# Optimization experiments

Hardware: AMD Instinct MI355X
Metric: run time of the kernel (lower is better)

The kernel has to match this reference:

```python
import jax, jax.numpy as jnp
import numpy as np

L_IN, L_FREQ, L_OUT = 128, 64, 64
C_IN, C_OUT, T_DIM = 64, 64, 256
SPIN = 1

# ---------- self-contained spin-weighted SHT (MW sampling), replacing s2fft ----------

def _mw_thetas(L, extended):
    n = 2 * L - 1 if extended else L
    return (2 * np.arange(n) + 1) * np.pi / (2 * L - 1)

def _wigner_d_stack(L, thetas, n):
    # d^l_{m,n}(theta) = <l,m| exp(-i theta Jy) |l,n>, computed via eigh of the
    # Hermitian angular-momentum operator Jy. Output (ntheta, L, 2L-1), m at col L-1+m.
    nth = len(thetas)
    out = np.zeros((nth, L, 2 * L - 1), dtype=np.float64)
    for l in range(abs(n), L):
        dim = 2 * l + 1
        m = np.arange(-l, l).astype(np.float64)
        ap = np.sqrt(l * (l + 1.0) - m * (m + 1.0))
        Jy = np.zeros((dim, dim), dtype=np.complex128)
        i = np.arange(dim - 1)
        Jy[i + 1, i] = -0.5j * ap
        Jy[i, i + 1] = 0.5j * ap
        lam, V = np.linalg.eigh(Jy)
        coeff = V * np.conj(V[l + n, :])[None, :]
        phases = np.exp(-1j * np.outer(lam, thetas))
        out[:, l, L - 1 - l:L + l] = (coeff @ phases).T.real
    return out

def _mw_quad_weights(L):
    # per-theta weights on the mirror-extended grid: q_t = (1/(2L-1)) sum_k w(k) e^{ik theta_t}
    # with w(k) = int_0^pi e^{ik t} sin(t) dt
    k = np.arange(-(L - 1), L)
    den = np.where(np.abs(k) == 1, 1, 1 - k * k).astype(np.float64)
    w = np.where(k % 2 == 0, 2.0 / den, 0.0).astype(np.complex128)
    w[k == 1] = 0.5j * np.pi
    w[k == -1] = -0.5j * np.pi
    th = _mw_thetas(L, True)
    return ((w[None, :] * np.exp(1j * np.outer(th, k))).sum(1) / (2 * L - 1)).real

# transform kernels are constants (built once at import, numpy)
_D_FWD = jnp.asarray(_wigner_d_stack(L_IN, _mw_thetas(L_IN, True), -SPIN) * _mw_quad_weights(L_IN)[:, None, None], jnp.float32)
_D_INV = jnp.asarray(_wigner_d_stack(L_OUT, _mw_thetas(L_OUT, False), -SPIN), jnp.float32)
_CL_IN = jnp.asarray(((-1.0) ** SPIN) * np.sqrt((2 * np.arange(L_IN) + 1) / (4 * np.pi)), jnp.float32)
_CL_OUT = jnp.asarray(((-1.0) ** SPIN) * np.sqrt((2 * np.arange(L_OUT) + 1) / (4 * np.pi)), jnp.float32)
_m_all = np.arange(-(L_IN - 1), L_IN)
_PARITY = jnp.asarray(np.where((_m_all + SPIN) % 2 == 0, 1.0, -1.0), jnp.float32)

def sht_forward(x):
    # x: (L_IN, 2*L_IN-1, C) real spatial -> flm: (L_IN, 2*L_IN-1, C) complex, m at L_IN-1+m
    nphi = 2 * L_IN - 1
    ftm = jnp.fft.fftshift(jnp.fft.fft(x, axis=1), axes=1) * (2 * jnp.pi / nphi)
    # mirror extension in theta with (-1)^(m+spin) parity (all channels at once)
    g_ext = jnp.concatenate([ftm, _PARITY[None, :, None] * ftm[::-1][1:]], axis=0)
    flm = jnp.einsum('tlm,tmc->lmc', _D_FWD, g_ext)
    return flm * _CL_IN[:, None, None]

def sht_inverse(flm):
    # flm: (L_OUT, 2*L_OUT-1, C) complex -> (L_OUT, 2*L_OUT-1, C) real spatial
    ftm = jnp.einsum('tlm,lmc->tmc', _D_INV, flm * _CL_OUT[:, None, None])
    return (jnp.fft.ifft(jnp.fft.ifftshift(ftm, axes=1), axis=1) * (2 * L_OUT - 1)).real

def resize_flm(flm, l_in, l_out):
    # centered truncation / zero-pad of (L, 2L-1, C) harmonic coefficients
    if l_out <= l_in:
        d = l_in - l_out
        return flm[:l_out, d:d + 2 * l_out - 1]
    d = l_out - l_in
    return jnp.pad(flm, ((0, d), (d, d), (0, 0)))

# ---------- inputs and parameters ----------

def setup_inputs():
    key = jax.random.key(0)
    ks = jax.random.split(key, 12)
    n = lambda i, shape, s: jax.random.normal(ks[i], shape, jnp.float32) * s
    return {
        'x': jax.random.normal(ks[0], (L_IN, 2 * L_IN - 1, C_IN), jnp.float32),
        't_emb': jax.random.normal(ks[1], (T_DIM,), jnp.float32),
        'spec_conv_w': n(2, (C_IN, C_OUT), (1.0 / C_IN) ** 0.5),
        'spec_conv_b': jnp.zeros((C_OUT,), jnp.float32),
        'spec_wr': n(3, (L_FREQ, C_IN, C_OUT), (0.5 / C_IN) ** 0.5),
        'spec_wi': n(4, (L_FREQ, C_IN, C_OUT), (0.5 / C_IN) ** 0.5),
        'spec_tr_w': n(5, (T_DIM, L_FREQ), (1.0 / T_DIM) ** 0.5),
        'spec_tr_b': jnp.zeros((L_FREQ,), jnp.float32),
        'spec_ti_w': n(6, (T_DIM, L_FREQ), (1.0 / T_DIM) ** 0.5),
        'spec_ti_b': jnp.zeros((L_FREQ,), jnp.float32),
        'spat_conv1_w': n(7, (C_IN, C_OUT), (1.0 / C_IN) ** 0.5),
        'spat_conv1_b': jnp.zeros((C_OUT,), jnp.float32),
        'spat_t_w': n(8, (T_DIM, 2 * C_OUT), (1.0 / T_DIM) ** 0.5),
        'spat_t_b': jnp.zeros((2 * C_OUT,), jnp.float32),
        'spat_weight': n(9, (C_OUT, C_OUT), 0.01),
        'spat_conv2_w': n(10, (C_OUT, C_OUT), (1.0 / C_OUT) ** 0.5),
        'spat_conv2_b': jnp.zeros((C_OUT,), jnp.float32),
        'ln_scale': jnp.ones((C_OUT,), jnp.float32),
        'ln_bias': jnp.zeros((C_OUT,), jnp.float32),
    }

def reference(x, t_emb, spec_conv_w, spec_conv_b, spec_wr, spec_wi, spec_tr_w, spec_tr_b, spec_ti_w, spec_ti_b, spat_conv1_w, spat_conv1_b, spat_t_w, spat_t_b, spat_weight, spat_conv2_w, spat_conv2_b, ln_scale, ln_bias):
    # ----- SphericalSpectralTimeConv branch -----
    flm = sht_forward(x)                                   # (L_IN, 2L_IN-1, C_IN) complex
    flm = resize_flm(flm, L_IN, L_FREQ)                    # (L_FREQ, 2L_FREQ-1, C_IN)
    conv_flm = jnp.einsum('lmi,io->lmo', flm, spec_conv_w) + spec_conv_b
    t_c = (t_emb @ spec_tr_w + spec_tr_b) + 1j * (t_emb @ spec_ti_w + spec_ti_b)   # (L_FREQ,)
    w = t_c[:, None, None] * (spec_wr + 1j * spec_wi)      # (L_FREQ, C_IN, C_OUT)
    flm = jnp.einsum('lmi,lio->lmo', flm, w) + conv_flm
    xs = sht_inverse(resize_flm(flm, L_FREQ, L_OUT))       # (L_OUT, 2L_OUT-1, C_OUT) real
    xs = xs / (jnp.linalg.norm(xs, axis=-1, keepdims=True) + 1e-6)
    # ----- SpatialTimeConv branch (path='down') -----
    h = jnp.einsum('lmi,io->lmo', x, spat_conv1_w) + spat_conv1_b
    t = t_emb @ spat_t_w + spat_t_b
    w_t, b_t = t[:C_OUT], t[C_OUT:]
    h = jnp.einsum('lmi,io->lmo', h, w_t[None, :] * spat_weight)
    h = sht_inverse(resize_flm(sht_forward(h), L_IN, L_OUT))
    h = jnp.einsum('lmi,io->lmo', h, spat_conv2_w) + spat_conv2_b + b_t
    # ----- combine: add, gelu, LayerNorm (eps=1e-6 over channels) -----
    y = jax.nn.gelu(xs + h)
    mu = jnp.mean(y, axis=-1, keepdims=True)
    var = jnp.var(y, axis=-1, keepdims=True)
    return (y - mu) * jax.lax.rsqrt(var + 1e-6) * ln_scale + ln_bias
```

## Files before the change

### kernel.cpp

```cpp
#include <hip/hip_runtime.h>
#include <math.h>

#define DPI 3.141592653589793238462643383279502884

__device__ __forceinline__ float wave_sum64(float v) {
#pragma unroll
  for (int off = 32; off > 0; off >>= 1) v += __shfl_xor(v, off, 64);
  return v;
}

__device__ __forceinline__ float gelu_tanh(float v) {
  float u = 0.7978845608028654f * (v + 0.044715f * v * v * v);
  return 0.5f * v * (1.0f + tanhf(u));
}

__global__ __launch_bounds__(256) void ct_setup(
    float* __restrict__ Deff, float* __restrict__ Dinv,
    float2* __restrict__ T255, float2* __restrict__ T127,
    const float* __restrict__ temb, const float* __restrict__ trw,
    const float* __restrict__ trb, const float* __restrict__ tiw,
    const float* __restrict__ tib, const float* __restrict__ stw,
    const float* __restrict__ stb, float* tcr, float* tci, float* tv) {
  int b = blockIdx.x;
  int tid = threadIdx.x;
  if (b >= 255) {
    if (b == 445) {
      if (tid < 64) {
        float ar = trb[tid], ai = tib[tid];
        for (int k = 0; k < 256; ++k) {
          float e = temb[k];
          ar = fmaf(e, trw[k * 64 + tid], ar);
          ai = fmaf(e, tiw[k * 64 + tid], ai);
        }
        tcr[tid] = ar; tci[tid] = ai;
      } else if (tid < 192) {
        int j = tid - 64;
        float a = stb[j];
        for (int k = 0; k < 256; ++k) a = fmaf(temb[k], stw[k * 128 + j], a);
        tv[j] = a;
      }
    } else {
      int id = (b - 255) * 256 + tid;
      if (id < 255 * 127) {
        int p = id / 127, mm = id % 127;
        double ang = 2.0 * DPI * (double)((mm - 63) * p) / 255.0;
        T255[id] = make_float2((float)cos(ang), (float)(-sin(ang)));
      }
      if (id < 127 * 127) {
        int mm = id / 127, p = id % 127;
        double ang = 2.0 * DPI * (double)((mm - 63) * p) / 127.0;
        T127[id] = make_float2((float)cos(ang), (float)sin(ang));
      }
    }
    return;
  }
  __shared__ double red[64];
  __shared__ float clf[64];
  int mode = (b < 128) ? 0 : 1;
  if (tid < 64)
    clf[tid] = (float)(-sqrt((2.0 * tid + 1.0) / (4.0 * DPI)));
  int t, mm;
  if (mode == 0) { t = b; mm = tid; }
  else { mm = b - 128; t = tid; }
  double denomN = (mode == 0) ? 255.0 : 127.0;
  double beta = (2.0 * t + 1.0) * DPI / denomN;
  float coeff;
  if (mode == 0) {
    if (tid < 63) {
      int k = 2 * (tid + 1);
      red[tid] = 8.0 * cos((double)k * beta) / (1.0 - (double)k * (double)k);
    } else if (tid == 63) {
      red[63] = 4.0;
    }
    __syncthreads();
    for (int s = 32; s > 0; s >>= 1) {
      if (tid < s) red[tid] += red[tid + s];
      __syncthreads();
    }
    double s = red[0] / 255.0;
    if (t == 127) s *= 0.5;
    coeff = (float)(s * (2.0 * DPI / 255.0));
    if (tid >= 127) return;
  } else {
    __syncthreads();
    coeff = 1.0f;
    if (tid >= 64) return;
  }
  int m = mm - 63;
  double cb = cos(beta);
  double ch = cos(0.5 * beta), sh = sin(0.5 * beta);
  int am = (m < 0) ? -m : m;
  int l0v = (am > 1) ? am : 1;
  double seed;
  if (m >= 1) {
    double j = (double)m;
    double K = exp(0.5 * (lgamma(2.0 * j + 1.0) - lgamma(j) - lgamma(j + 2.0)));
    double sgn = ((m + 1) & 1) ? -1.0 : 1.0;
    seed = sgn * K * pow(ch, j - 1.0) * pow(sh, j + 1.0);
  } else if (m <= -1) {
    double j = (double)(-m);
    double K = exp(0.5 * (lgamma(2.0 * j + 1.0) - lgamma(j) - lgamma(j + 2.0)));
    seed = K * pow(ch, j + 1.0) * pow(sh, j - 1.0);
  } else {
    seed = -sqrt(2.0) * sh * ch;
  }
  float dl = (float)seed, dm1 = 0.0f, S_cur = 0.0f;
  float cbf = (float)cb, mf = (float)m;
  for (int l = 0; l < 64; ++l) {
    float val = 0.0f;
    if (l >= l0v) {
      val = dl * coeff * clf[l];
      float Ld = (float)l, lp = Ld + 1.0f;
      float S_next = sqrtf((lp * lp - mf * mf) * (lp * lp - 1.0f));
      float num1 = (2.0f * Ld + 1.0f) * (Ld * lp * cbf + mf);
      float dn = (num1 * dl - lp * S_cur * dm1) / (Ld * S_next);
      dm1 = dl; dl = dn; S_cur = S_next;
    }
    if (mode == 0) Deff[((size_t)t * 127 + mm) * 64 + l] = val;
    else Dinv[((size_t)mm * 64 + l) * 64 + t] = val;
  }
}

__global__ void ct_AM(const float* __restrict__ cw, const float* __restrict__ wr,
                      const float* __restrict__ wi, const float* __restrict__ tcr,
                      const float* __restrict__ tci, const float* __restrict__ c1w,
                      const float* __restrict__ c1b, const float* __restrict__ sw,
                      const float* __restrict__ tv, const float* __restrict__ Deff,
                      float2* __restrict__ A2, float* __restrict__ Mm,
                      float* __restrict__ bias2, float* __restrict__ Sl) {
  int b = blockIdx.x, o = threadIdx.x;
  if (b < 64) {
    int l = b;
    float tr = tcr[l], ti = tci[l];
    for (int i = 0; i < 64; ++i) {
      int idx = (l * 64 + i) * 64 + o;
      float r = wr[idx], s = wi[idx];
      A2[idx] = make_float2(cw[i * 64 + o] + tr * r - ti * s, tr * s + ti * r);
    }
  } else if (b < 128) {
    int j = b - 64;
    float wt = tv[o];
    float acc = 0.f;
    for (int i = 0; i < 64; ++i) acc = fmaf(c1w[j * 64 + i], sw[i * 64 + o], acc);
    Mm[j * 64 + o] = wt * acc;
    if (j == 0) {
      float bb = 0.f;
      for (int i = 0; i < 64; ++i) bb = fmaf(c1b[i], sw[i * 64 + o], bb);
      bias2[o] = wt * bb;
    }
  } else {
    int l = o;
    float s = 0.f;
    for (int t = 0; t < 128; ++t) s += Deff[((size_t)t * 127 + 63) * 64 + l];
    Sl[l] = s;
  }
}

__global__ __launch_bounds__(256) void ct_dft(const float* __restrict__ x,
                                              const float2* __restrict__ T255,
                                              float* __restrict__ Are, float* __restrict__ Aim,
                                              float* __restrict__ Bre, float* __restrict__ Bim) {
  __shared__ float xs_[64][64];
  __shared__ float tsr[64][64], tsi[64][64];
  int t = blockIdx.x, mh = blockIdx.y, ph = blockIdx.z;
  float* ore = ph ? Bre : Are;
  float* oim = ph ? Bim : Aim;
  int pbase = ph * 128;
  int Ktot = ph ? 127 : 128;
  int tid = threadIdx.x;
  int cg = tid & 15, mg = tid >> 4;
  float accr[4][4], acci[4][4];
#pragma unroll
  for (int j = 0; j < 4; ++j)
#pragma unroll
    for (int q = 0; q < 4; ++q) { accr[j][q] = 0.f; acci[j][q] = 0.f; }
  for (int k0 = 0; k0 < Ktot; k0 += 64) {
    int kn = (Ktot - k0 < 64) ? Ktot - k0 : 64;
    __syncthreads();
    {
      int r = tid >> 2, c4 = (tid & 3) * 16;
      if (r < kn) {
        const float4* src = (const float4*)(x + ((size_t)t * 255 + pbase + k0 + r) * 64 + c4);
        float4* dst = (float4*)&xs_[r][c4];
        dst[0] = src[0]; dst[1] = src[1]; dst[2] = src[2]; dst[3] = src[3];
      }
    }
    for (int e = tid; e < 64 * 64; e += 256) {
      int r = e >> 6, mi = e & 63;
      if (r < kn) {
        int gcol = mh * 64 + mi; if (gcol > 126) gcol = 126;
        float2 tw = T255[(size_t)(pbase + k0 + r) * 127 + gcol];
        tsr[r][mi] = tw.x; tsi[r][mi] = tw.y;
      }
    }
    __syncthreads();
#pragma unroll 4
    for (int k = 0; k < kn; ++k) {
      float4 xv = *(const float4*)&xs_[k][cg * 4];
      float4 tr4 = *(const float4*)&tsr[k][mg * 4];
      float4 ti4 = *(const float4*)&tsi[k][mg * 4];
      float xv4[4] = {xv.x, xv.y, xv.z, xv.w};
      float trv[4] = {tr4.x, tr4.y, tr4.z, tr4.w};
      float tiv[4] = {ti4.x, ti4.y, ti4.z, ti4.w};
#pragma unroll
      for (int j = 0; j < 4; ++j)
#pragma unroll
        for (int q = 0; q < 4; ++q) {
          accr[j][q] = fmaf(xv4[q], trv[j], accr[j][q]);
          acci[j][q] = fmaf(xv4[q], tiv[j], acci[j][q]);
        }
    }
  }
#pragma unroll
  for (int j = 0; j < 4; ++j) {
    int gmm = mh * 64 + mg * 4 + j;
    if (gmm > 126) continue;
    size_t ob = ((size_t)t * 127 + gmm) * 64 + cg * 4;
    *(float4*)(ore + ob) = make_float4(accr[j][0], accr[j][1], accr[j][2], accr[j][3]);
    *(float4*)(oim + ob) = make_float4(acci[j][0], acci[j][1], acci[j][2], acci[j][3]);
  }
}

__global__ __launch_bounds__(256) void ct_projf(const float* __restrict__ Deff,
                                                const float* __restrict__ fAre,
                                                const float* __restrict__ fAim,
                                                const float* __restrict__ fBre,
                                                const float* __restrict__ fBim,
                                                float* __restrict__ flmA_re, float* __restrict__ flmA_im,
                                                float* __restrict__ flmB_re, float* __restrict__ flmB_im) {
  __shared__ float Dsh[64][32];
  __shared__ float fr_[64][64], fi_[64][64];
  int mm = blockIdx.x, lh = blockIdx.y, th = blockIdx.z;
  float* ore = th ? flmB_re : flmA_re;
  float* oim = th ? flmB_im : flmA_im;
  int tb = th * 64;
  int tid = threadIdx.x;
  int cg = tid & 15, lg = tid >> 4;
  for (int e = tid; e < 64 * 32; e += 256) {
    int r = e >> 5, li = e & 31;
    Dsh[r][li] = Deff[((size_t)(tb + r) * 127 + mm) * 64 + lh * 32 + li];
  }
  for (int e = tid; e < 64 * 64; e += 256) {
    int r = e >> 6, c = e & 63;
    size_t idx = ((size_t)(tb + r) * 127 + mm) * 64 + c;
    fr_[r][c] = fAre[idx] + fBre[idx];
    fi_[r][c] = fAim[idx] + fBim[idx];
  }
  __syncthreads();
  float ar[2][4], ai[2][4];
#pragma unroll
  for (int li = 0; li < 2; ++li)
#pragma unroll
    for (int q = 0; q < 4; ++q) { ar[li][q] = 0.f; ai[li][q] = 0.f; }
#pragma unroll 4
  for (int k = 0; k < 64; ++k) {
    float4 fr4 = *(const float4*)&fr_[k][cg * 4];
    float4 fi4 = *(const float4*)&fi_[k][cg * 4];
    float2 d2 = *(const float2*)&Dsh[k][lg * 2];
    float frv[4] = {fr4.x, fr4.y, fr4.z, fr4.w};
    float fiv[4] = {fi4.x, fi4.y, fi4.z, fi4.w};
    float dv[2] = {d2.x, d2.y};
#pragma unroll
    for (int li = 0; li < 2; ++li)
#pragma unroll
      for (int q = 0; q < 4; ++q) {
        ar[li][q] = fmaf(dv[li], frv[q], ar[li][q]);
        ai[li][q] = fmaf(dv[li], fiv[q], ai[li][q]);
      }
  }
#pragma unroll
  for (int li = 0; li < 2; ++li) {
    size_t row = ((size_t)mm * 64 + lh * 32 + lg * 2 + li) * 64 + cg * 4;
    *(float4*)(ore + row) = make_float4(ar[li][0], ar[li][1], ar[li][2], ar[li][3]);
    *(float4*)(oim + row) = make_float4(ai[li][0], ai[li][1], ai[li][2], ai[li][3]);
  }
}

__global__ __launch_bounds__(256) void ct_mix(const float* __restrict__ flmA_re,
                                              const float* __restrict__ flmA_im,
                                              const float* __restrict__ flmB_re,
                                              const float* __restrict__ flmB_im,
                                              const float2* __restrict__ A2,
                                              const float* __restrict__ Mm,
                                              const float* __restrict__ scb,
                                              const float* __restrict__ bias2,
                                              const float* __restrict__ Sl,
                                              float* __restrict__ s_re, float* __restrict__ s_im,
                                              float* __restrict__ h_re, float* __restrict__ h_im) {
  __shared__ float Ar_[64][32], Ai_[64][32], Msh[64][32];
  __shared__ float Br_[64][65], Bi_[64][65];
  int l = blockIdx.x, mh = blockIdx.y, oh = blockIdx.z;
  int tid = threadIdx.x;
  int og = tid & 15, mg = tid >> 4;
  for (int e = tid; e < 64 * 32; e += 256) {
    int r = e >> 5, oi = e & 31;
    float2 a = A2[((size_t)l * 64 + r) * 64 + oh * 32 + oi];
    Ar_[r][oi] = a.x; Ai_[r][oi] = a.y;
    Msh[r][oi] = Mm[r * 64 + oh * 32 + oi];
  }
  for (int e = tid; e < 64 * 64; e += 256) {
    int mi = e >> 6, i = e & 63;
    int gmm = mh * 64 + mi; if (gmm > 126) gmm = 126;
    size_t idx = ((size_t)gmm * 64 + l) * 64 + i;
    Br_[mi][i] = flmA_re[idx] + flmB_re[idx];
    Bi_[mi][i] = flmA_im[idx] + flmB_im[idx];
  }
  __syncthreads();
  int o0 = oh * 32 + og * 2;
  float b0[2] = {scb[o0], scb[o0 + 1]};
  float sr[4][2], si[4][2], hr[4][2], hi[4][2];
#pragma unroll
  for (int jm = 0; jm < 4; ++jm)
#pragma unroll
    for (int qo = 0; qo < 2; ++qo) {
      sr[jm][qo] = b0[qo]; si[jm][qo] = 0.f; hr[jm][qo] = 0.f; hi[jm][qo] = 0.f;
    }
#pragma unroll 4
  for (int k = 0; k < 64; ++k) {
    float2 ar2 = *(const float2*)&Ar_[k][og * 2];
    float2 ai2 = *(const float2*)&Ai_[k][og * 2];
    float2 mv2 = *(const float2*)&Msh[k][og * 2];
    float br4[4], bi4[4];
#pragma unroll
    for (int jm = 0; jm < 4; ++jm) {
      br4[jm] = Br_[mg * 4 + jm][k];
      bi4[jm] = Bi_[mg * 4 + jm][k];
    }
    float arv[2] = {ar2.x, ar2.y}, aiv[2] = {ai2.x, ai2.y}, mvv[2] = {mv2.x, mv2.y};
#pragma unroll
    for (int jm = 0; jm < 4; ++jm)
#pragma unroll
      for (int qo = 0; qo < 2; ++qo) {
        sr[jm][qo] = fmaf(br4[jm], arv[qo], sr[jm][qo]);
        sr[jm][qo] = fmaf(-bi4[jm], aiv[qo], sr[jm][qo]);
        si[jm][qo] = fmaf(br4[jm], aiv[qo], si[jm][qo]);
        si[jm][qo] = fmaf(bi4[jm], arv[qo], si[jm][qo]);
        hr[jm][qo] = fmaf(br4[jm], mvv[qo], hr[jm][qo]);
        hi[jm][qo] = fmaf(bi4[jm], mvv[qo], hi[jm][qo]);
      }
  }
  float Slv = Sl[l];
  float bb[2] = {bias2[o0], bias2[o0 + 1]};
#pragma unroll
  for (int jm = 0; jm < 4; ++jm) {
    int gmm = mh * 64 + mg * 4 + jm;
    if (gmm > 126) continue;
    if (gmm == 63) {
#pragma unroll
      for (int qo = 0; qo < 2; ++qo)
        hr[jm][qo] = fmaf(255.0f * Slv, bb[qo], hr[jm][qo]);
    }
    size_t row = ((size_t)gmm * 64 + l) * 64 + o0;
    *(float2*)(s_re + row) = make_float2(sr[jm][0], sr[jm][1]);
    *(float2*)(s_im + row) = make_float2(si[jm][0], si[jm][1]);
    *(float2*)(h_re + row) = make_float2(hr[jm][0], hr[jm][1]);
    *(float2*)(h_im + row) = make_float2(hi[jm][0], hi[jm][1]);
  }
}

__global__ __launch_bounds__(256) void ct_proji(const float* __restrict__ Dinv,
                                                const float* __restrict__ s_re,
                                                const float* __restrict__ s_im,
                                                const float* __restrict__ h_re,
                                                const float* __restrict__ h_im,
                                                float* __restrict__ fos_re, float* __restrict__ fos_im,
                                                float* __restrict__ foh_re, float* __restrict__ foh_im) {
  __shared__ float Dsh[64][64];
  __shared__ float Br_[64][32], Bi_[64][32];
  int mm = blockIdx.x, br = blockIdx.y, ch = blockIdx.z;
  const float* ire = br ? h_re : s_re;
  const float* iim = br ? h_im : s_im;
  float* ore = br ? foh_re : fos_re;
  float* oim = br ? foh_im : fos_im;
  int tid = threadIdx.x;
  int cg = tid & 15, tg = tid >> 4;
  for (int e = tid; e < 64 * 64; e += 256) {
    int r = e >> 6, tt = e & 63;
    Dsh[r][tt] = Dinv[((size_t)mm * 64 + r) * 64 + tt];
  }
  for (int e = tid; e < 64 * 32; e += 256) {
    int r = e >> 5, cc = e & 31;
    size_t idx = ((size_t)mm * 64 + r) * 64 + ch * 32 + cc;
    Br_[r][cc] = ire[idx];
    Bi_[r][cc] = iim[idx];
  }
  __syncthreads();
  float ar[4][2], ai[4][2];
#pragma unroll
  for (int j = 0; j < 4; ++j)
#pragma unroll
    for (int q = 0; q < 2; ++q) { ar[j][q] = 0.f; ai[j][q] = 0.f; }
#pragma unroll 4
  for (int k = 0; k < 64; ++k) {
    float4 d4 = *(const float4*)&Dsh[k][tg * 4];
    float2 fr2 = *(const float2*)&Br_[k][cg * 2];
    float2 fi2 = *(const float2*)&Bi_[k][cg * 2];
    float dv[4] = {d4.x, d4.y, d4.z, d4.w};
    float frv[2] = {fr2.x, fr2.y}, fiv[2] = {fi2.x, fi2.y};
#pragma unroll
    for (int j = 0; j < 4; ++j)
#pragma unroll
      for (int q = 0; q < 2; ++q) {
        ar[j][q] = fmaf(dv[j], frv[q], ar[j][q]);
        ai[j][q] = fmaf(dv[j], fiv[q], ai[j][q]);
      }
  }
#pragma unroll
  for (int j = 0; j < 4; ++j) {
    int t = tg * 4 + j;
    size_t ob = ((size_t)t * 127 + mm) * 64 + ch * 32 + cg * 2;
    *(float2*)(ore + ob) = make_float2(ar[j][0], ar[j][1]);
    *(float2*)(oim + ob) = make_float2(ai[j][0], ai[j][1]);
  }
}

__global__ __launch_bounds__(256) void ct_idft(const float2* __restrict__ T127,
                                               const float* __restrict__ fos_re,
                                               const float* __restrict__ fos_im,
                                               const float* __restrict__ foh_re,
                                               const float* __restrict__ foh_im,
                                               float* __restrict__ xsbA, float* __restrict__ xsbB,
                                               float* __restrict__ hsbA, float* __restrict__ hsbB) {
  __shared__ float Ar_[32][64], Ai_[32][64], Br_[32][64], Bi_[32][64];
  int t = blockIdx.x, br = blockIdx.y;
  int z = blockIdx.z;
  int ph = z >> 1, kh = z & 1;
  const float* fre = br ? foh_re : fos_re;
  const float* fim = br ? foh_im : fos_im;
  float* outp = br ? (kh ? hsbB : hsbA) : (kh ? xsbB : xsbA);
  int kbase = kh * 64;
  int Ktot = kh ? 63 : 64;
  int tid = threadIdx.x;
  int cg = tid & 15, pg = tid >> 4;
  float acc[4][4];
#pragma unroll
  for (int j = 0; j < 4; ++j)
#pragma unroll
    for (int q = 0; q < 4; ++q) acc[j][q] = 0.f;
  for (int k0 = 0; k0 < Ktot; k0 += 32) {
    int kn = (Ktot - k0 < 32) ? Ktot - k0 : 32;
    __syncthreads();
    for (int e = tid; e < 32 * 64; e += 256) {
      int r = e >> 6, j = e & 63;
      if (r < kn) {
        int gmm = kbase + k0 + r;
        int gp = ph * 64 + j; if (gp > 126) gp = 126;
        float2 tw = T127[(size_t)gmm * 127 + gp];
        Ar_[r][j] = tw.x; Ai_[r][j] = tw.y;
        size_t bidx = ((size_t)t * 127 + gmm) * 64 + j;
        Br_[r][j] = fre[bidx]; Bi_[r][j] = fim[bidx];
      }
    }
    __syncthreads();
#pragma unroll 4
    for (int k = 0; k < kn; ++k) {
      float4 a_r = *(const float4*)&Ar_[k][pg * 4];
      float4 a_i = *(const float4*)&Ai_[k][pg * 4];
      float4 b_r = *(const float4*)&Br_[k][cg * 4];
      float4 b_i = *(const float4*)&Bi_[k][cg * 4];
      float arv[4] = {a_r.x, a_r.y, a_r.z, a_r.w};
      float aiv[4] = {a_i.x, a_i.y, a_i.z, a_i.w};
      float brv[4] = {b_r.x, b_r.y, b_r.z, b_r.w};
      float biv[4] = {b_i.x, b_i.y, b_i.z, b_i.w};
#pragma unroll
      for (int j = 0; j < 4; ++j)
#pragma unroll
        for (int q = 0; q < 4; ++q) {
          acc[j][q] = fmaf(brv[q], arv[j], acc[j][q]);
          acc[j][q] = fmaf(biv[q], -aiv[j], acc[j][q]);
        }
    }
  }
#pragma unroll
  for (int j = 0; j < 4; ++j) {
    int gp = ph * 64 + pg * 4 + j;
    if (gp > 126) continue;
    *(float4*)(outp + ((size_t)t * 127 + gp) * 64 + cg * 4) =
        make_float4(acc[j][0], acc[j][1], acc[j][2], acc[j][3]);
  }
}

__global__ __launch_bounds__(256) void ct_fin(const float* __restrict__ xsbA,
                                              const float* __restrict__ xsbB,
                                              const float* __restrict__ hsbA,
                                              const float* __restrict__ hsbB,
                                              const float* __restrict__ c2w,
                                              const float* __restrict__ c2b,
                                              const float* __restrict__ tv,
                                              const float* __restrict__ lns,
                                              const float* __restrict__ lnb,
                                              float* __restrict__ out) {
  int w = threadIdx.x >> 6, lane = threadIdx.x & 63;
  size_t row = (size_t)blockIdx.x * 4 + w;
  size_t base = row * 64 + lane;
  float hv = hsbA[base] + hsbB[base];
  float xv = xsbA[base] + xsbB[base];
  float acc = c2b[lane] + tv[64 + lane];
#pragma unroll 16
  for (int i = 0; i < 64; ++i)
    acc = fmaf(__shfl(hv, i, 64), c2w[i * 64 + lane], acc);
  float ss = wave_sum64(xv * xv);
  xv = xv / (sqrtf(ss) + 1e-6f);
  float y = xv + acc;
  float g = gelu_tanh(y);
  float mu = wave_sum64(g) * (1.0f / 64.0f);
  float d = g - mu;
  float var = wave_sum64(d * d) * (1.0f / 64.0f);
  out[base] = d * rsqrtf(var + 1e-6f) * lns[lane] + lnb[lane];
}

extern "C" void kernel_launch(void* const* d_in, const int* in_sizes, int n_in,
                              void* d_out, int out_size, void* d_ws, size_t ws_size,
                              hipStream_t stream) {
  const float* x = (const float*)d_in[0];
  const float* temb = (const float*)d_in[1];
  const float* scw = (const float*)d_in[2];
  const float* scb = (const float*)d_in[3];
  const float* swr = (const float*)d_in[4];
  const float* swi = (const float*)d_in[5];
  const float* strw = (const float*)d_in[6];
  const float* strb = (const float*)d_in[7];
  const float* stiw = (const float*)d_in[8];
  const float* stib = (const float*)d_in[9];
  const float* c1w = (const float*)d_in[10];
  const float* c1b = (const float*)d_in[11];
  const float* stw = (const float*)d_in[12];
  const float* stb = (const float*)d_in[13];
  const float* sweight = (const float*)d_in[14];
  const float* c2w = (const float*)d_in[15];
  const float* c2b = (const float*)d_in[16];
  const float* lns = (const float*)d_in[17];
  const float* lnb = (const float*)d_in[18];
  float* out = (float*)d_out;

  char* base = (char*)d_ws;
  size_t off = 0;
  auto alloc = [&](size_t bytes) -> void* {
    void* p = base + off;
    off += (bytes + 255) & ~(size_t)255;
    return p;
  };
  float* tcr = (float*)alloc(64 * sizeof(float));
  float* tci = (float*)alloc(64 * sizeof(float));
  float* tv = (float*)alloc(128 * sizeof(float));
  float* Mm = (float*)alloc(4096 * sizeof(float));
  float* bias2 = (float*)alloc(64 * sizeof(float));
  float* Sl = (float*)alloc(64 * sizeof(float));
  float2* A2 = (float2*)alloc(262144 * sizeof(float2));
  float* Deff = (float*)alloc(1040384 * sizeof(float));
  float* Dinv = (float*)alloc(520192 * sizeof(float));
  float2* T255 = (float2*)alloc(32385 * sizeof(float2));
  float2* T127 = (float2*)alloc(16129 * sizeof(float2));
  float* ftmA_re = (float*)alloc(1040384 * sizeof(float));
  float* ftmA_im = (float*)alloc(1040384 * sizeof(float));
  float* ftmB_re = (float*)alloc(1040384 * sizeof(float));
  float* ftmB_im = (float*)alloc(1040384 * sizeof(float));
  float* flmA_re = (float*)alloc(520192 * sizeof(float));
  float* flmA_im = (float*)alloc(520192 * sizeof(float));
  float* flmB_re = (float*)alloc(520192 * sizeof(float));
  float* flmB_im = (float*)alloc(520192 * sizeof(float));
  if (off > ws_size) return;
  float* s_re = ftmA_re;
  float* s_im = ftmA_im;
  float* h_re = ftmB_re;
  float* h_im = ftmB_im;
  float* fos_re = Deff;
  float* fos_im = Deff + 520192;
  float* foh_re = flmA_re;
  float* foh_im = flmA_im;
  float* xsbA = flmB_re;
  float* xsbB = flmB_im;
  float* hsbA = ftmA_re;
  float* hsbB = ftmA_im;

  hipLaunchKernelGGL(ct_setup, dim3(446), dim3(256), 0, stream, Deff, Dinv, T255, T127,
                     temb, strw, strb, stiw, stib, stw, stb, tcr, tci, tv);
  hipLaunchKernelGGL(ct_AM, dim3(129), dim3(64), 0, stream, scw, swr, swi, tcr, tci,
                     c1w, c1b, sweight, tv, Deff, A2, Mm, bias2, Sl);
  hipLaunchKernelGGL(ct_dft, dim3(128, 2, 2), dim3(256), 0, stream, x, T255,
                     ftmA_re, ftmA_im, ftmB_re, ftmB_im);
  hipLaunchKernelGGL(ct_projf, dim3(127, 2, 2), dim3(256), 0, stream, Deff,
                     ftmA_re, ftmA_im, ftmB_re, ftmB_im,
                     flmA_re, flmA_im, flmB_re, flmB_im);
  hipLaunchKernelGGL(ct_mix, dim3(64, 2, 2), dim3(256), 0, stream,
                     flmA_re, flmA_im, flmB_re, flmB_im, A2, Mm, scb, bias2, Sl,
                     s_re, s_im, h_re, h_im);
  hipLaunchKernelGGL(ct_proji, dim3(127, 2, 2), dim3(256), 0, stream, Dinv,
                     s_re, s_im, h_re, h_im, fos_re, fos_im, foh_re, foh_im);
  hipLaunchKernelGGL(ct_idft, dim3(64, 2, 4), dim3(256), 0, stream, T127,
                     fos_re, fos_im, foh_re, foh_im, xsbA, xsbB, hsbA, hsbB);
  hipLaunchKernelGGL(ct_fin, dim3(2032), dim3(256), 0, stream, xsbA, xsbB, hsbA, hsbB,
                     c2w, c2b, tv, lns, lnb, out);
}
```

Before: 206.9 us.

## Fold weight-prep kernel into setup and compute DFT twiddles on the fly

```diff
diff --git a/kernel.cpp b/kernel.cpp
--- a/kernel.cpp
+++ b/kernel.cpp
@@ -14,51 +14,83 @@
   return 0.5f * v * (1.0f + tanhf(u));
 }
 
+#define CN255F ((float)(-2.0 * DPI / 255.0))
+#define CN127F ((float)(2.0 * DPI / 127.0))
+
 __global__ __launch_bounds__(256) void ct_setup(
     float* __restrict__ Deff, float* __restrict__ Dinv,
-    float2* __restrict__ T255, float2* __restrict__ T127,
     const float* __restrict__ temb, const float* __restrict__ trw,
     const float* __restrict__ trb, const float* __restrict__ tiw,
     const float* __restrict__ tib, const float* __restrict__ stw,
-    const float* __restrict__ stb, float* tcr, float* tci, float* tv) {
+    const float* __restrict__ stb, const float* __restrict__ scw,
+    const float* __restrict__ swr, const float* __restrict__ swi,
+    const float* __restrict__ c1w, const float* __restrict__ c1b,
+    const float* __restrict__ sweight,
+    float2* __restrict__ A2, float* __restrict__ Mm,
+    float* __restrict__ bias2, float* __restrict__ tv) {
+  __shared__ double red[64];
+  __shared__ float clf[64];
+  __shared__ float fb1[256];
+  __shared__ float fb2[256];
   int b = blockIdx.x;
   int tid = threadIdx.x;
   if (b >= 255) {
-    if (b == 445) {
-      if (tid < 64) {
-        float ar = trb[tid], ai = tib[tid];
-        for (int k = 0; k < 256; ++k) {
-          float e = temb[k];
-          ar = fmaf(e, trw[k * 64 + tid], ar);
-          ai = fmaf(e, tiw[k * 64 + tid], ai);
-        }
-        tcr[tid] = ar; tci[tid] = ai;
-      } else if (tid < 192) {
-        int j = tid - 64;
-        float a = stb[j];
-        for (int k = 0; k < 256; ++k) a = fmaf(temb[k], stw[k * 128 + j], a);
-        tv[j] = a;
+    if (b < 319) {
+      int l = b - 255;
+      fb1[tid] = temb[tid] * trw[tid * 64 + l];
+      fb2[tid] = temb[tid] * tiw[tid * 64 + l];
+      __syncthreads();
+      for (int s = 128; s > 0; s >>= 1) {
+        if (tid < s) { fb1[tid] += fb1[tid + s]; fb2[tid] += fb2[tid + s]; }
+        __syncthreads();
+      }
+      float tr = fb1[0] + trb[l], ti = fb2[0] + tib[l];
+      int o = tid & 63, iq = tid >> 6;
+      for (int i = iq * 16; i < iq * 16 + 16; ++i) {
+        int idx = (l * 64 + i) * 64 + o;
+        float r = swr[idx], s2 = swi[idx];
+        A2[idx] = make_float2(scw[i * 64 + o] + tr * r - ti * s2, tr * s2 + ti * r);
+      }
+    } else if (b < 383) {
+      int j = b - 319;
+      int o = tid & 63, part = tid >> 6;
+      float p = 0.f;
+      for (int k = part * 64; k < part * 64 + 64; ++k)
+        p = fmaf(temb[k], stw[k * 128 + o], p);
+      fb1[part * 64 + o] = p;
+      __syncthreads();
+      if (part == 0) fb2[o] = fb1[o] + fb1[64 + o] + fb1[128 + o] + fb1[192 + o] + stb[o];
+      __syncthreads();
+      float tvo = fb2[o];
+      float q = 0.f;
+      for (int i = part * 16; i < part * 16 + 16; ++i)
+        q = fmaf(c1w[j * 64 + i], sweight[i * 64 + o], q);
+      __syncthreads();
+      fb1[part * 64 + o] = q;
+      __syncthreads();
+      if (part == 0) Mm[j * 64 + o] = tvo * (fb1[o] + fb1[64 + o] + fb1[128 + o] + fb1[192 + o]);
+      if (j == 0) {
+        float bq = 0.f;
+        for (int i = part * 16; i < part * 16 + 16; ++i)
+          bq = fmaf(c1b[i], sweight[i * 64 + o], bq);
+        __syncthreads();
+        fb1[part * 64 + o] = bq;
+        __syncthreads();
+        if (part == 0) bias2[o] = tvo * (fb1[o] + fb1[64 + o] + fb1[128 + o] + fb1[192 + o]);
       }
     } else {
-      int id = (b - 255) * 256 + tid;
-      if (id < 255 * 127) {
-        int p = id / 127, mm = id % 127;
-        double ang = 2.0 * DPI * (double)((mm - 63) * p) / 255.0;
-        T255[id] = make_float2((float)cos(ang), (float)(-sin(ang)));
-      }
-      if (id < 127 * 127) {
-        int mm = id / 127, p = id % 127;
-        double ang = 2.0 * DPI * (double)((mm - 63) * p) / 127.0;
-        T127[id] = make_float2((float)cos(ang), (float)sin(ang));
-      }
+      int o = tid & 127, part = tid >> 7;
+      float p = 0.f;
+      for (int k = part * 128; k < part * 128 + 128; ++k)
+        p = fmaf(temb[k], stw[k * 128 + o], p);
+      fb1[part * 128 + o] = p;
+      __syncthreads();
+      if (part == 0) tv[o] = fb1[o] + fb1[128 + o] + stb[o];
     }
     return;
   }
-  __shared__ double red[64];
-  __shared__ float clf[64];
   int mode = (b < 128) ? 0 : 1;
-  if (tid < 64)
-    clf[tid] = (float)(-sqrt((2.0 * tid + 1.0) / (4.0 * DPI)));
+  if (tid < 64) clf[tid] = (float)(-sqrt((2.0 * tid + 1.0) / (4.0 * DPI)));
   int t, mm;
   if (mode == 0) { t = b; mm = tid; }
   else { mm = b - 128; t = tid; }
@@ -121,43 +153,7 @@
   }
 }
 
-__global__ void ct_AM(const float* __restrict__ cw, const float* __restrict__ wr,
-                      const float* __restrict__ wi, const float* __restrict__ tcr,
-                      const float* __restrict__ tci, const float* __restrict__ c1w,
-                      const float* __restrict__ c1b, const float* __restrict__ sw,
-                      const float* __restrict__ tv, const float* __restrict__ Deff,
-                      float2* __restrict__ A2, float* __restrict__ Mm,
-                      float* __restrict__ bias2, float* __restrict__ Sl) {
-  int b = blockIdx.x, o = threadIdx.x;
-  if (b < 64) {
-    int l = b;
-    float tr = tcr[l], ti = tci[l];
-    for (int i = 0; i < 64; ++i) {
-      int idx = (l * 64 + i) * 64 + o;
-      float r = wr[idx], s = wi[idx];
-      A2[idx] = make_float2(cw[i * 64 + o] + tr * r - ti * s, tr * s + ti * r);
-    }
-  } else if (b < 128) {
-    int j = b - 64;
-    float wt = tv[o];
-    float acc = 0.f;
-    for (int i = 0; i < 64; ++i) acc = fmaf(c1w[j * 64 + i], sw[i * 64 + o], acc);
-    Mm[j * 64 + o] = wt * acc;
-    if (j == 0) {
-      float bb = 0.f;
-      for (int i = 0; i < 64; ++i) bb = fmaf(c1b[i], sw[i * 64 + o], bb);
-      bias2[o] = wt * bb;
-    }
-  } else {
-    int l = o;
-    float s = 0.f;
-    for (int t = 0; t < 128; ++t) s += Deff[((size_t)t * 127 + 63) * 64 + l];
-    Sl[l] = s;
-  }
-}
-
 __global__ __launch_bounds__(256) void ct_dft(const float* __restrict__ x,
-                                              const float2* __restrict__ T255,
                                               float* __restrict__ Are, float* __restrict__ Aim,
                                               float* __restrict__ Bre, float* __restrict__ Bim) {
   __shared__ float xs_[64][64];
@@ -168,7 +164,7 @@
   int pbase = ph * 128;
   int Ktot = ph ? 127 : 128;
   int tid = threadIdx.x;
-  int cg = tid & 15, mg = tid >> 4;
+  int cg_ = tid & 15, mg = tid >> 4;
   float accr[4][4], acci[4][4];
 #pragma unroll
   for (int j = 0; j < 4; ++j)
@@ -189,14 +185,17 @@
       int r = e >> 6, mi = e & 63;
       if (r < kn) {
         int gcol = mh * 64 + mi; if (gcol > 126) gcol = 126;
-        float2 tw = T255[(size_t)(pbase + k0 + r) * 127 + gcol];
-        tsr[r][mi] = tw.x; tsi[r][mi] = tw.y;
+        int p = pbase + k0 + r;
+        float ang = CN255F * (float)((gcol - 63) * p);
+        float sv, cv;
+        __sincosf(ang, &sv, &cv);
+        tsr[r][mi] = cv; tsi[r][mi] = sv;
       }
     }
     __syncthreads();
 #pragma unroll 4
     for (int k = 0; k < kn; ++k) {
-      float4 xv = *(const float4*)&xs_[k][cg * 4];
+      float4 xv = *(const float4*)&xs_[k][cg_ * 4];
       float4 tr4 = *(const float4*)&tsr[k][mg * 4];
       float4 ti4 = *(const float4*)&tsi[k][mg * 4];
       float xv4[4] = {xv.x, xv.y, xv.z, xv.w};
@@ -215,7 +214,7 @@
   for (int j = 0; j < 4; ++j) {
     int gmm = mh * 64 + mg * 4 + j;
     if (gmm > 126) continue;
-    size_t ob = ((size_t)t * 127 + gmm) * 64 + cg * 4;
+    size_t ob = ((size_t)t * 127 + gmm) * 64 + cg_ * 4;
     *(float4*)(ore + ob) = make_float4(accr[j][0], accr[j][1], accr[j][2], accr[j][3]);
     *(float4*)(oim + ob) = make_float4(acci[j][0], acci[j][1], acci[j][2], acci[j][3]);
   }
@@ -235,7 +234,7 @@
   float* oim = th ? flmB_im : flmA_im;
   int tb = th * 64;
   int tid = threadIdx.x;
-  int cg = tid & 15, lg = tid >> 4;
+  int cg_ = tid & 15, lg = tid >> 4;
   for (int e = tid; e < 64 * 32; e += 256) {
     int r = e >> 5, li = e & 31;
     Dsh[r][li] = Deff[((size_t)(tb + r) * 127 + mm) * 64 + lh * 32 + li];
@@ -254,8 +253,8 @@
     for (int q = 0; q < 4; ++q) { ar[li][q] = 0.f; ai[li][q] = 0.f; }
 #pragma unroll 4
   for (int k = 0; k < 64; ++k) {
-    float4 fr4 = *(const float4*)&fr_[k][cg * 4];
-    float4 fi4 = *(const float4*)&fi_[k][cg * 4];
+    float4 fr4 = *(const float4*)&fr_[k][cg_ * 4];
+    float4 fi4 = *(const float4*)&fi_[k][cg_ * 4];
     float2 d2 = *(const float2*)&Dsh[k][lg * 2];
     float frv[4] = {fr4.x, fr4.y, fr4.z, fr4.w};
     float fiv[4] = {fi4.x, fi4.y, fi4.z, fi4.w};
@@ -270,7 +269,7 @@
   }
 #pragma unroll
   for (int li = 0; li < 2; ++li) {
-    size_t row = ((size_t)mm * 64 + lh * 32 + lg * 2 + li) * 64 + cg * 4;
+    size_t row = ((size_t)mm * 64 + lh * 32 + lg * 2 + li) * 64 + cg_ * 4;
     *(float4*)(ore + row) = make_float4(ar[li][0], ar[li][1], ar[li][2], ar[li][3]);
     *(float4*)(oim + row) = make_float4(ai[li][0], ai[li][1], ai[li][2], ai[li][3]);
   }
@@ -284,18 +283,26 @@
                                               const float* __restrict__ Mm,
                                               const float* __restrict__ scb,
                                               const float* __restrict__ bias2,
-                                              const float* __restrict__ Sl,
+                                              const float* __restrict__ Deff,
                                               float* __restrict__ s_re, float* __restrict__ s_im,
                                               float* __restrict__ h_re, float* __restrict__ h_im) {
   __shared__ float Ar_[64][32], Ai_[64][32], Msh[64][32];
   __shared__ float Br_[64][65], Bi_[64][65];
+  __shared__ float rb[256];
   int l = blockIdx.x, mh = blockIdx.y, oh = blockIdx.z;
   int tid = threadIdx.x;
   int og = tid & 15, mg = tid >> 4;
+  rb[tid] = (mh == 0 && tid < 128) ? Deff[((size_t)tid * 127 + 63) * 64 + l] : 0.f;
+  __syncthreads();
+  for (int s = 128; s > 0; s >>= 1) {
+    if (tid < s) rb[tid] += rb[tid + s];
+    __syncthreads();
+  }
+  float slv = rb[0];
   for (int e = tid; e < 64 * 32; e += 256) {
     int r = e >> 5, oi = e & 31;
-    float2 a = A2[((size_t)l * 64 + r) * 64 + oh * 32 + oi];
-    Ar_[r][oi] = a.x; Ai_[r][oi] = a.y;
+    float2 aa = A2[((size_t)l * 64 + r) * 64 + oh * 32 + oi];
+    Ar_[r][oi] = aa.x; Ai_[r][oi] = aa.y;
     Msh[r][oi] = Mm[r * 64 + oh * 32 + oi];
   }
   for (int e = tid; e < 64 * 64; e += 256) {
@@ -339,7 +346,6 @@
         hi[jm][qo] = fmaf(bi4[jm], mvv[qo], hi[jm][qo]);
       }
   }
-  float Slv = Sl[l];
   float bb[2] = {bias2[o0], bias2[o0 + 1]};
 #pragma unroll
   for (int jm = 0; jm < 4; ++jm) {
@@ -348,7 +354,7 @@
     if (gmm == 63) {
 #pragma unroll
       for (int qo = 0; qo < 2; ++qo)
-        hr[jm][qo] = fmaf(255.0f * Slv, bb[qo], hr[jm][qo]);
+        hr[jm][qo] = fmaf(255.0f * slv, bb[qo], hr[jm][qo]);
     }
     size_t row = ((size_t)gmm * 64 + l) * 64 + o0;
     *(float2*)(s_re + row) = make_float2(sr[jm][0], sr[jm][1]);
@@ -373,7 +379,7 @@
   float* ore = br ? foh_re : fos_re;
   float* oim = br ? foh_im : fos_im;
   int tid = threadIdx.x;
-  int cg = tid & 15, tg = tid >> 4;
+  int cg_ = tid & 15, tg = tid >> 4;
   for (int e = tid; e < 64 * 64; e += 256) {
     int r = e >> 6, tt = e & 63;
     Dsh[r][tt] = Dinv[((size_t)mm * 64 + r) * 64 + tt];
@@ -393,8 +399,8 @@
 #pragma unroll 4
   for (int k = 0; k < 64; ++k) {
     float4 d4 = *(const float4*)&Dsh[k][tg * 4];
-    float2 fr2 = *(const float2*)&Br_[k][cg * 2];
-    float2 fi2 = *(const float2*)&Bi_[k][cg * 2];
+    float2 fr2 = *(const float2*)&Br_[k][cg_ * 2];
+    float2 fi2 = *(const float2*)&Bi_[k][cg_ * 2];
     float dv[4] = {d4.x, d4.y, d4.z, d4.w};
     float frv[2] = {fr2.x, fr2.y}, fiv[2] = {fi2.x, fi2.y};
 #pragma unroll
@@ -408,14 +414,13 @@
 #pragma unroll
   for (int j = 0; j < 4; ++j) {
     int t = tg * 4 + j;
-    size_t ob = ((size_t)t * 127 + mm) * 64 + ch * 32 + cg * 2;
+    size_t ob = ((size_t)t * 127 + mm) * 64 + ch * 32 + cg_ * 2;
     *(float2*)(ore + ob) = make_float2(ar[j][0], ar[j][1]);
     *(float2*)(oim + ob) = make_float2(ai[j][0], ai[j][1]);
   }
 }
 
-__global__ __launch_bounds__(256) void ct_idft(const float2* __restrict__ T127,
-                                               const float* __restrict__ fos_re,
+__global__ __launch_bounds__(256) void ct_idft(const float* __restrict__ fos_re,
                                                const float* __restrict__ fos_im,
                                                const float* __restrict__ foh_re,
                                                const float* __restrict__ foh_im,
@@ -431,7 +436,7 @@
   int kbase = kh * 64;
   int Ktot = kh ? 63 : 64;
   int tid = threadIdx.x;
-  int cg = tid & 15, pg = tid >> 4;
+  int cg_ = tid & 15, pg = tid >> 4;
   float acc[4][4];
 #pragma unroll
   for (int j = 0; j < 4; ++j)
@@ -445,8 +450,10 @@
       if (r < kn) {
         int gmm = kbase + k0 + r;
         int gp = ph * 64 + j; if (gp > 126) gp = 126;
-        float2 tw = T127[(size_t)gmm * 127 + gp];
-        Ar_[r][j] = tw.x; Ai_[r][j] = tw.y;
+        float ang = CN127F * (float)((gmm - 63) * gp);
+        float sv, cv;
+        __sincosf(ang, &sv, &cv);
+        Ar_[r][j] = cv; Ai_[r][j] = sv;
         size_t bidx = ((size_t)t * 127 + gmm) * 64 + j;
         Br_[r][j] = fre[bidx]; Bi_[r][j] = fim[bidx];
       }
@@ -456,8 +463,8 @@
     for (int k = 0; k < kn; ++k) {
       float4 a_r = *(const float4*)&Ar_[k][pg * 4];
       float4 a_i = *(const float4*)&Ai_[k][pg * 4];
-      float4 b_r = *(const float4*)&Br_[k][cg * 4];
-      float4 b_i = *(const float4*)&Bi_[k][cg * 4];
+      float4 b_r = *(const float4*)&Br_[k][cg_ * 4];
+      float4 b_i = *(const float4*)&Bi_[k][cg_ * 4];
       float arv[4] = {a_r.x, a_r.y, a_r.z, a_r.w};
       float aiv[4] = {a_i.x, a_i.y, a_i.z, a_i.w};
       float brv[4] = {b_r.x, b_r.y, b_r.z, b_r.w};
@@ -475,7 +482,7 @@
   for (int j = 0; j < 4; ++j) {
     int gp = ph * 64 + pg * 4 + j;
     if (gp > 126) continue;
-    *(float4*)(outp + ((size_t)t * 127 + gp) * 64 + cg * 4) =
+    *(float4*)(outp + ((size_t)t * 127 + gp) * 64 + cg_ * 4) =
         make_float4(acc[j][0], acc[j][1], acc[j][2], acc[j][3]);
   }
 }
@@ -540,17 +547,12 @@
     off += (bytes + 255) & ~(size_t)255;
     return p;
   };
-  float* tcr = (float*)alloc(64 * sizeof(float));
-  float* tci = (float*)alloc(64 * sizeof(float));
   float* tv = (float*)alloc(128 * sizeof(float));
   float* Mm = (float*)alloc(4096 * sizeof(float));
   float* bias2 = (float*)alloc(64 * sizeof(float));
-  float* Sl = (float*)alloc(64 * sizeof(float));
   float2* A2 = (float2*)alloc(262144 * sizeof(float2));
   float* Deff = (float*)alloc(1040384 * sizeof(float));
   float* Dinv = (float*)alloc(520192 * sizeof(float));
-  float2* T255 = (float2*)alloc(32385 * sizeof(float2));
-  float2* T127 = (float2*)alloc(16129 * sizeof(float2));
   float* ftmA_re = (float*)alloc(1040384 * sizeof(float));
   float* ftmA_im = (float*)alloc(1040384 * sizeof(float));
   float* ftmB_re = (float*)alloc(1040384 * sizeof(float));
@@ -573,21 +575,20 @@
   float* hsbA = ftmA_re;
   float* hsbB = ftmA_im;
 
-  hipLaunchKernelGGL(ct_setup, dim3(446), dim3(256), 0, stream, Deff, Dinv, T255, T127,
-                     temb, strw, strb, stiw, stib, stw, stb, tcr, tci, tv);
-  hipLaunchKernelGGL(ct_AM, dim3(129), dim3(64), 0, stream, scw, swr, swi, tcr, tci,
-                     c1w, c1b, sweight, tv, Deff, A2, Mm, bias2, Sl);
-  hipLaunchKernelGGL(ct_dft, dim3(128, 2, 2), dim3(256), 0, stream, x, T255,
+  hipLaunchKernelGGL(ct_setup, dim3(384), dim3(256), 0, stream, Deff, Dinv,
+                     temb, strw, strb, stiw, stib, stw, stb,
+                     scw, swr, swi, c1w, c1b, sweight, A2, Mm, bias2, tv);
+  hipLaunchKernelGGL(ct_dft, dim3(128, 2, 2), dim3(256), 0, stream, x,
                      ftmA_re, ftmA_im, ftmB_re, ftmB_im);
   hipLaunchKernelGGL(ct_projf, dim3(127, 2, 2), dim3(256), 0, stream, Deff,
                      ftmA_re, ftmA_im, ftmB_re, ftmB_im,
                      flmA_re, flmA_im, flmB_re, flmB_im);
   hipLaunchKernelGGL(ct_mix, dim3(64, 2, 2), dim3(256), 0, stream,
-                     flmA_re, flmA_im, flmB_re, flmB_im, A2, Mm, scb, bias2, Sl,
+                     flmA_re, flmA_im, flmB_re, flmB_im, A2, Mm, scb, bias2, Deff,
                      s_re, s_im, h_re, h_im);
   hipLaunchKernelGGL(ct_proji, dim3(127, 2, 2), dim3(256), 0, stream, Dinv,
                      s_re, s_im, h_re, h_im, fos_re, fos_im, foh_re, foh_im);
-  hipLaunchKernelGGL(ct_idft, dim3(64, 2, 4), dim3(256), 0, stream, T127,
+  hipLaunchKernelGGL(ct_idft, dim3(64, 2, 4), dim3(256), 0, stream,
                      fos_re, fos_im, foh_re, foh_im, xsbA, xsbB, hsbA, hsbB);
   hipLaunchKernelGGL(ct_fin, dim3(2032), dim3(256), 0, stream, xsbA, xsbB, hsbA, hsbB,
                      c2w, c2b, tv, lns, lnb, out);
```

Measured after the change: 211.9 us. +2.4%, slower.
